# Kernel tuning notes

Hardware: AMD Instinct MI355X
Metric: run time of the kernel (lower is better)

The kernel has to match this reference:

```python
import jax, jax.numpy as jnp
import numpy as np

N_QUBITS = 7
N_LAYERS = 4
DIM = 2 ** N_QUBITS  # 128


def _cnot_perm(c, t, n=N_QUBITS):
    # PennyLane convention: wire 0 is the most-significant bit of the state index.
    idx = np.arange(2 ** n)
    ctrl = (idx >> (n - 1 - c)) & 1
    flipped = idx ^ (1 << (n - 1 - t))
    return np.where(ctrl == 1, flipped, idx)

# StronglyEntanglingLayers with a single layer uses range r=1: CNOT(j, (j+1) % n)
CNOT_PERMS = tuple(jnp.asarray(_cnot_perm(j, (j + 1) % N_QUBITS)) for j in range(N_QUBITS))

_bits = (np.arange(DIM)[None, :] >> (N_QUBITS - 1 - np.arange(N_QUBITS)[:, None])) & 1
Z_SIGNS = jnp.asarray(1.0 - 2.0 * _bits, dtype=jnp.float32)  # (7,128): +1 if wire bit 0 else -1


def _apply_1q(state, U, q):
    # state: (B,128) complex; U: (B,2,2) batched or (2,2) shared
    B = state.shape[0]
    s = state.reshape(B, 2 ** q, 2, 2 ** (N_QUBITS - 1 - q))
    if U.ndim == 3:
        s = jnp.einsum('bij,bpjq->bpiq', U, s)
    else:
        s = jnp.einsum('ij,bpjq->bpiq', U, s)
    return s.reshape(B, DIM)


def _simulate(x, weights):
    # x: (B,7) angles; weights: (4,7,3) Rot params. Returns <Z_q> per wire: (B,7)
    B = x.shape[0]
    state = jnp.zeros((B, DIM), jnp.complex64).at[:, 0].set(1.0)
    half = 0.5 * x
    c = jnp.cos(half).astype(jnp.complex64)  # (B,7)
    s = jnp.sin(half).astype(jnp.complex64)
    for l in range(N_LAYERS):
        # AngleEmbedding: RX(x_j) on wire j (data re-uploading, same x each block)
        for q in range(N_QUBITS):
            cq, sq = c[:, q], s[:, q]
            U = jnp.stack([jnp.stack([cq, -1j * sq], axis=-1),
                           jnp.stack([-1j * sq, cq], axis=-1)], axis=-2)  # (B,2,2)
            state = _apply_1q(state, U, q)
        # StronglyEntanglingLayers single layer: Rot(phi,theta,omega) per wire
        for q in range(N_QUBITS):
            phi, theta, omega = weights[l, q, 0], weights[l, q, 1], weights[l, q, 2]
            ct = jnp.cos(0.5 * theta).astype(jnp.complex64)
            st = jnp.sin(0.5 * theta).astype(jnp.complex64)
            ep = jnp.exp(-0.5j * (phi + omega).astype(jnp.complex64))
            em = jnp.exp(-0.5j * (phi - omega).astype(jnp.complex64))
            # Rot = RZ(omega) @ RY(theta) @ RZ(phi)
            U = jnp.stack([jnp.stack([ep * ct, -jnp.conj(em) * st]),
                           jnp.stack([em * st, jnp.conj(ep) * ct])])  # (2,2)
            state = _apply_1q(state, U, q)
        # entangler: CNOT(j, j+1 mod 7) for all j
        for q in range(N_QUBITS):
            state = state[:, CNOT_PERMS[q]]
    probs = state.real ** 2 + state.imag ** 2  # (B,128)
    return probs @ Z_SIGNS.T  # (B,7)


def setup_inputs() -> dict:
    key = jax.random.key(0)
    ks = jax.random.split(key, 6)
    B, n_classes = 16384, 22
    return {
        'x': jax.random.uniform(ks[0], (B, N_QUBITS), jnp.float32),
        'weights': jax.random.normal(ks[1], (N_LAYERS, N_QUBITS, 3), jnp.float32),
        'fc1_w': jax.random.normal(ks[2], (32, N_QUBITS), jnp.float32) * 0.3,
        'fc1_b': jax.random.normal(ks[3], (32,), jnp.float32) * 0.1,
        'fc2_w': jax.random.normal(ks[4], (n_classes, 32), jnp.float32) * 0.2,
        'fc2_b': jax.random.normal(ks[5], (n_classes,), jnp.float32) * 0.1,
    }


def reference(x, weights, fc1_w, fc1_b, fc2_w, fc2_b):
    q_out = _simulate(x, weights)                      # (B,7)
    h = jax.nn.relu(q_out @ fc1_w.T + fc1_b)           # (B,32); dropout is inference no-op
    return h @ fc2_w.T + fc2_b                         # (B,n_classes)
```

## Files before the change

### kernel.cpp

```cpp
#include <hip/hip_runtime.h>

constexpr int NQ = 7;
constexpr int NL = 4;
constexpr int NG = NL * NQ;
constexpr int NCLS = 22;
constexpr int EPB = 16;

typedef float v2 __attribute__((ext_vector_type(2)));
#define FMA2(a,b,c) __builtin_elementwise_fma((a),(b),(c))

__device__ __forceinline__ v2 sp(float s) { v2 r; r.x = s; r.y = s; return r; }
__device__ __forceinline__ v2 sel(bool c, v2 a, v2 b) {
    v2 r; r.x = c ? a.x : b.x; r.y = c ? a.y : b.y; return r;
}

template<int CTRL>
__device__ __forceinline__ float fdpp(float v) {
    return __int_as_float(__builtin_amdgcn_mov_dpp(__float_as_int(v), CTRL, 0xF, 0xF, true));
}
template<int OFF>
__device__ __forceinline__ float fswz(float v) {
    return __int_as_float(__builtin_amdgcn_ds_swizzle(__float_as_int(v), OFF));
}
template<int M>
__device__ __forceinline__ float xorl(float v) {
    if      constexpr (M == 1)  return fdpp<0xB1>(v);
    else if constexpr (M == 2)  return fdpp<0x4E>(v);
    else if constexpr (M == 4)  return fswz<0x101F>(v);
    else                        return fdpp<0x128>(v);
}
template<int M>
__device__ __forceinline__ v2 shufv(v2 v) {
    v2 r; r.x = xorl<M>(v.x); r.y = xorl<M>(v.y); return r;
}

__device__ __forceinline__ void fuse(const float* __restrict__ u, float c, float s,
                                     float4& A, float4& B) {
    A.x = fmaf(c, u[0],  s * u[3]);  A.y = fmaf(c, u[1], -s * u[2]);
    A.z = fmaf(c, u[2],  s * u[1]);  A.w = fmaf(c, u[3], -s * u[0]);
    B.x = fmaf(c, u[4],  s * u[7]);  B.y = fmaf(c, u[5], -s * u[6]);
    B.z = fmaf(c, u[6],  s * u[5]);  B.w = fmaf(c, u[7], -s * u[4]);
}

template<int M>
__device__ __forceinline__ void gateLane(int lane, float4 A, float4 B,
                                         v2 X[4], v2 Y[4]) {
    const bool hi = (lane & M) != 0;
    const float cvr = hi ? B.z : A.x, cvi = hi ? B.w : A.y;
    const float cwr = hi ? B.x : A.z, cwi = hi ? B.y : A.w;
    v2 Xs[4], Ys[4];
    #pragma unroll
    for (int j = 0; j < 4; ++j) { Xs[j] = shufv<M>(X[j]); Ys[j] = shufv<M>(Y[j]); }
    #pragma unroll
    for (int j = 0; j < 4; ++j) {
        v2 nX = FMA2(sp(cvr), X[j], FMA2(sp(-cvi), Y[j], FMA2(sp(cwr), Xs[j], sp(-cwi)*Ys[j])));
        v2 nY = FMA2(sp(cvr), Y[j], FMA2(sp( cvi), X[j], FMA2(sp(cwr), Ys[j], sp( cwi)*Xs[j])));
        X[j] = nX; Y[j] = nY;
    }
}

__device__ __forceinline__ void gateCross(float4 A, float4 B,
                                          v2& Xa, v2& Ya, v2& Xb, v2& Yb) {
    v2 nXa = FMA2(sp(A.x), Xa, FMA2(sp(-A.y), Ya, FMA2(sp(A.z), Xb, sp(-A.w)*Yb)));
    v2 nYa = FMA2(sp(A.x), Ya, FMA2(sp( A.y), Xa, FMA2(sp(A.z), Yb, sp( A.w)*Xb)));
    v2 nXb = FMA2(sp(B.x), Xa, FMA2(sp(-B.y), Ya, FMA2(sp(B.z), Xb, sp(-B.w)*Yb)));
    v2 nYb = FMA2(sp(B.x), Ya, FMA2(sp( B.y), Xa, FMA2(sp(B.z), Yb, sp( B.w)*Xb)));
    Xa = nXa; Ya = nYa; Xb = nXb; Yb = nYb;
}

__global__ __launch_bounds__(256) void reupload_kernel(
    const float* __restrict__ x,
    const float* __restrict__ wts,
    const float* __restrict__ fc1_w,
    const float* __restrict__ fc1_b,
    const float* __restrict__ fc2_w,
    const float* __restrict__ fc2_b,
    float* __restrict__ out,
    int B)
{
    __shared__ __align__(16) float rotU[NG * 8];
    __shared__ float2 csb[EPB * NQ];
    __shared__ __align__(16) float fU[NG * EPB * 8];
    __shared__ __align__(16) float fUT[NL * EPB * 8];
    __shared__ __align__(16) float hbuf[EPB][32];

    const int tid = threadIdx.x;
    if (tid < EPB * NQ) {
        const int e = tid / NQ, q = tid % NQ;
        const int bb = blockIdx.x * EPB + e;
        const float xv = (bb < B) ? x[bb*NQ + q] : 0.f;
        const float h = 0.5f * xv;
        csb[tid] = make_float2(__cosf(h), __sinf(h));
    } else if (tid >= 128 && tid < 128 + NG) {
        const int g = tid - 128;
        float phi = wts[g*3+0], th = wts[g*3+1], om = wts[g*3+2];
        float ct = __cosf(0.5f*th), st = __sinf(0.5f*th);
        float ap = 0.5f*(phi+om),  am = 0.5f*(phi-om);
        float cp = __cosf(ap), sp_ = __sinf(ap);
        float cm = __cosf(am), sm = __sinf(am);
        float* u = &rotU[g*8];
        u[0] =  cp*ct; u[1] = -sp_*ct;
        u[2] = -cm*st; u[3] = -sm*st;
        u[4] =  cm*st; u[5] = -sm*st;
        u[6] =  cp*ct; u[7] =  sp_*ct;
    }
    __syncthreads();
    #pragma unroll
    for (int i = tid; i < NG * EPB; i += 256) {
        const int g = i >> 4, e = i & 15;
        const int q = g % NQ;
        const float2 cs = csb[e*NQ + q];
        float4 A, Bq;
        fuse(&rotU[g*8], cs.x, cs.y, A, Bq);
        float4* dst = reinterpret_cast<float4*>(&fU[(g*EPB + e)*8]);
        dst[0] = A; dst[1] = Bq;
        if (q == 5) {
            const int l = g / NQ;
            float* td = &fUT[(l*EPB + e)*8];
            td[0] = A.x; td[1] = Bq.x; td[2] = A.y; td[3] = Bq.y;
            td[4] = A.z; td[5] = Bq.z; td[6] = A.w; td[7] = Bq.w;
        }
    }
    __syncthreads();

    const int lane = threadIdx.x & 63;
    const int u    = threadIdx.x & 15;
    const int grp  = threadIdx.x >> 4;
    const int b    = blockIdx.x * EPB + grp;
    if (b >= B) return;

    const int srcLane = (lane & 48) | ((u ^ (u >> 1)) & 15);

    v2 X[4], Y[4];
    #pragma unroll
    for (int j = 0; j < 4; ++j) { X[j] = sp(0.f); Y[j] = sp(0.f); }
    X[0].x = (u == 0) ? 1.f : 0.f;

    #pragma unroll
    for (int l = 0; l < NL; ++l) {
        float4 A, Bq;
        #define LOADU(q) { const float4* up = reinterpret_cast<const float4*>( \
            &fU[((l*NQ + (q))*EPB + grp)*8]); A = up[0]; Bq = up[1]; }
        LOADU(0); gateLane<8>(lane, A, Bq, X, Y);
        LOADU(1); gateLane<4>(lane, A, Bq, X, Y);
        LOADU(2); gateLane<2>(lane, A, Bq, X, Y);
        LOADU(3); gateLane<1>(lane, A, Bq, X, Y);
        LOADU(4);
        gateCross(A, Bq, X[0], Y[0], X[2], Y[2]);
        gateCross(A, Bq, X[1], Y[1], X[3], Y[3]);
        {
            const v2* tp = reinterpret_cast<const v2*>(&fUT[(l*EPB + grp)*8]);
            const v2 c00r = tp[0], c00i = tp[1], c01r = tp[2], c01i = tp[3];
            #pragma unroll
            for (int j = 0; j < 4; ++j) {
                const v2 Xxx = X[j].xx, Xyy = X[j].yy;
                const v2 Yxx = Y[j].xx, Yyy = Y[j].yy;
                v2 nX = FMA2(c00r, Xxx, FMA2(-c00i, Yxx, FMA2(c01r, Xyy, (-c01i)*Yyy)));
                v2 nY = FMA2(c00r, Yxx, FMA2( c00i, Xxx, FMA2(c01r, Yyy, ( c01i)*Xyy)));
                X[j] = nX; Y[j] = nY;
            }
        }
        LOADU(6);
        gateCross(A, Bq, X[0], Y[0], X[1], Y[1]);
        gateCross(A, Bq, X[2], Y[2], X[3], Y[3]);
        #undef LOADU

        #pragma unroll
        for (int j = 0; j < 4; ++j) {
            X[j].x = __shfl(X[j].x, srcLane); X[j].y = __shfl(X[j].y, srcLane);
            Y[j].x = __shfl(Y[j].x, srcLane); Y[j].y = __shfl(Y[j].y, srcLane);
        }
        {
            const bool cc = (lane & 1) != 0;
            v2 t;
            t = X[0]; X[0] = sel(cc, X[2], X[0]); X[2] = sel(cc, t, X[2]);
            t = X[1]; X[1] = sel(cc, X[3], X[1]); X[3] = sel(cc, t, X[3]);
            t = Y[0]; Y[0] = sel(cc, Y[2], Y[0]); Y[2] = sel(cc, t, Y[2]);
            t = Y[1]; Y[1] = sel(cc, Y[3], Y[1]); Y[3] = sel(cc, t, Y[3]);
        }
        {
            X[2] = X[2].yx; X[3] = X[3].yx; Y[2] = Y[2].yx; Y[3] = Y[3].yx;
        }
        {
            float t;
            t = X[0].y; X[0].y = X[1].y; X[1].y = t;
            t = X[2].y; X[2].y = X[3].y; X[3].y = t;
            t = Y[0].y; Y[0].y = Y[1].y; Y[1].y = t;
            t = Y[2].y; Y[2].y = Y[3].y; Y[3].y = t;
        }
        {
            X[1] = shufv<8>(X[1]); X[3] = shufv<8>(X[3]);
            Y[1] = shufv<8>(Y[1]); Y[3] = shufv<8>(Y[3]);
        }
    }

    v2 P[4];
    #pragma unroll
    for (int j = 0; j < 4; ++j) P[j] = FMA2(X[j], X[j], Y[j]*Y[j]);
    const v2 Sa = P[0] + P[1], Sb = P[2] + P[3];
    const v2 Se = P[0] + P[2], So = P[1] + P[3];
    const v2 T  = Sa + Sb;
    const float t = T.x + T.y;
    float z[NQ];
    z[0] = (lane & 8) ? -t : t;
    z[1] = (lane & 4) ? -t : t;
    z[2] = (lane & 2) ? -t : t;
    z[3] = (lane & 1) ? -t : t;
    z[4] = (Sa.x + Sa.y) - (Sb.x + Sb.y);
    z[5] = T.x - T.y;
    z[6] = (Se.x + Se.y) - (So.x + So.y);
    #pragma unroll
    for (int j = 0; j < NQ; ++j) {
        float v = z[j];
        v += xorl<1>(v);
        v += xorl<2>(v);
        const float q4  = fdpp<0x124>(v);
        const float q8  = fdpp<0x128>(v);
        const float q12 = fdpp<0x12C>(v);
        z[j] = (v + q8) + (q4 + q12);
    }

    float acc1a = fc1_b[u], acc1b = fc1_b[u + 16];
    #pragma unroll
    for (int j = 0; j < NQ; ++j) {
        acc1a = fmaf(z[j], fc1_w[u*NQ + j], acc1a);
        acc1b = fmaf(z[j], fc1_w[(u+16)*NQ + j], acc1b);
    }
    hbuf[grp][u]      = fmaxf(acc1a, 0.f);
    hbuf[grp][u + 16] = fmaxf(acc1b, 0.f);
    __builtin_amdgcn_wave_barrier();
    asm volatile("s_waitcnt lgkmcnt(0)" ::: "memory");
    __builtin_amdgcn_sched_barrier(0);

    float hv[32];
    #pragma unroll
    for (int i = 0; i < 8; ++i) {
        float4 v4 = *reinterpret_cast<const float4*>(&hbuf[grp][i*4]);
        hv[i*4+0] = v4.x; hv[i*4+1] = v4.y; hv[i*4+2] = v4.z; hv[i*4+3] = v4.w;
    }
    const int kb = (u < NCLS - 16) ? (u + 16) : 0;
    float acc2a = fc2_b[u], acc2b = fc2_b[kb];
    const float4* w4a = reinterpret_cast<const float4*>(fc2_w + u*32);
    const float4* w4b = reinterpret_cast<const float4*>(fc2_w + kb*32);
    #pragma unroll
    for (int i = 0; i < 8; ++i) {
        float4 wa = w4a[i], wb = w4b[i];
        acc2a = fmaf(hv[i*4+0], wa.x, acc2a); acc2b = fmaf(hv[i*4+0], wb.x, acc2b);
        acc2a = fmaf(hv[i*4+1], wa.y, acc2a); acc2b = fmaf(hv[i*4+1], wb.y, acc2b);
        acc2a = fmaf(hv[i*4+2], wa.z, acc2a); acc2b = fmaf(hv[i*4+2], wb.z, acc2b);
        acc2a = fmaf(hv[i*4+3], wa.w, acc2a); acc2b = fmaf(hv[i*4+3], wb.w, acc2b);
    }
    out[b*NCLS + u] = acc2a;
    if (u < NCLS - 16) out[b*NCLS + 16 + u] = acc2b;
}

extern "C" void kernel_launch(void* const* d_in, const int* in_sizes, int n_in,
                              void* d_out, int out_size, void* d_ws, size_t ws_size,
                              hipStream_t stream) {
    const float* x     = (const float*)d_in[0];
    const float* wts   = (const float*)d_in[1];
    const float* fc1_w = (const float*)d_in[2];
    const float* fc1_b = (const float*)d_in[3];
    const float* fc2_w = (const float*)d_in[4];
    const float* fc2_b = (const float*)d_in[5];
    float* out = (float*)d_out;

    const int B = in_sizes[0] / NQ;
    const int grid = (B + EPB - 1) / EPB;
    reupload_kernel<<<grid, 256, 0, stream>>>(x, wts, fc1_w, fc1_b, fc2_w, fc2_b, out, B);
}
```

Before: 20.12 us.

## Spread each 128-amplitude state over 32 lanes instead of 16

Each batch element's statevector now spans 32 lanes with 4 amplitudes per lane, down from 16 lanes with 8 amplitudes. Qubit 4 becomes a lane-level gate using a swizzle, the entangler permutation is adapted to 32 lanes, and the readout and MLP stages each use one output per lane. Blocks handle 8 elements, and a launch-bounds occupancy hint is added. This cuts per-thread register state and serial FMA chains in exchange for twice the threads per element, more cross-lane shuffles, and double the blocks with their per-block setup.

```diff
diff --git a/kernel.cpp b/kernel.cpp
--- a/kernel.cpp
+++ b/kernel.cpp
@@ -4,15 +4,12 @@
 constexpr int NL = 4;
 constexpr int NG = NL * NQ;
 constexpr int NCLS = 22;
-constexpr int EPB = 16;
+constexpr int EPB = 8;
 
 typedef float v2 __attribute__((ext_vector_type(2)));
 #define FMA2(a,b,c) __builtin_elementwise_fma((a),(b),(c))
 
 __device__ __forceinline__ v2 sp(float s) { v2 r; r.x = s; r.y = s; return r; }
-__device__ __forceinline__ v2 sel(bool c, v2 a, v2 b) {
-    v2 r; r.x = c ? a.x : b.x; r.y = c ? a.y : b.y; return r;
-}
 
 template<int CTRL>
 __device__ __forceinline__ float fdpp(float v) {
@@ -27,7 +24,8 @@
     if      constexpr (M == 1)  return fdpp<0xB1>(v);
     else if constexpr (M == 2)  return fdpp<0x4E>(v);
     else if constexpr (M == 4)  return fswz<0x101F>(v);
-    else                        return fdpp<0x128>(v);
+    else if constexpr (M == 8)  return fdpp<0x128>(v);
+    else                        return fswz<0x401F>(v);
 }
 template<int M>
 __device__ __forceinline__ v2 shufv(v2 v) {
@@ -44,15 +42,15 @@
 
 template<int M>
 __device__ __forceinline__ void gateLane(int lane, float4 A, float4 B,
-                                         v2 X[4], v2 Y[4]) {
+                                         v2 X[2], v2 Y[2]) {
     const bool hi = (lane & M) != 0;
     const float cvr = hi ? B.z : A.x, cvi = hi ? B.w : A.y;
     const float cwr = hi ? B.x : A.z, cwi = hi ? B.y : A.w;
-    v2 Xs[4], Ys[4];
-    #pragma unroll
-    for (int j = 0; j < 4; ++j) { Xs[j] = shufv<M>(X[j]); Ys[j] = shufv<M>(Y[j]); }
-    #pragma unroll
-    for (int j = 0; j < 4; ++j) {
+    v2 Xs[2], Ys[2];
+    #pragma unroll
+    for (int j = 0; j < 2; ++j) { Xs[j] = shufv<M>(X[j]); Ys[j] = shufv<M>(Y[j]); }
+    #pragma unroll
+    for (int j = 0; j < 2; ++j) {
         v2 nX = FMA2(sp(cvr), X[j], FMA2(sp(-cvi), Y[j], FMA2(sp(cwr), Xs[j], sp(-cwi)*Ys[j])));
         v2 nY = FMA2(sp(cvr), Y[j], FMA2(sp( cvi), X[j], FMA2(sp(cwr), Ys[j], sp( cwi)*Xs[j])));
         X[j] = nX; Y[j] = nY;
@@ -68,7 +66,7 @@
     Xa = nXa; Ya = nYa; Xb = nXb; Yb = nYb;
 }
 
-__global__ __launch_bounds__(256) void reupload_kernel(
+__global__ __launch_bounds__(256, 8) void reupload_kernel(
     const float* __restrict__ x,
     const float* __restrict__ wts,
     const float* __restrict__ fc1_w,
@@ -91,8 +89,8 @@
         const float xv = (bb < B) ? x[bb*NQ + q] : 0.f;
         const float h = 0.5f * xv;
         csb[tid] = make_float2(__cosf(h), __sinf(h));
-    } else if (tid >= 128 && tid < 128 + NG) {
-        const int g = tid - 128;
+    } else if (tid >= 64 && tid < 64 + NG) {
+        const int g = tid - 64;
         float phi = wts[g*3+0], th = wts[g*3+1], om = wts[g*3+2];
         float ct = __cosf(0.5f*th), st = __sinf(0.5f*th);
         float ap = 0.5f*(phi+om),  am = 0.5f*(phi-om);
@@ -105,9 +103,8 @@
         u[6] =  cp*ct; u[7] =  sp_*ct;
     }
     __syncthreads();
-    #pragma unroll
-    for (int i = tid; i < NG * EPB; i += 256) {
-        const int g = i >> 4, e = i & 15;
+    if (tid < NG * EPB) {
+        const int g = tid >> 3, e = tid & 7;
         const int q = g % NQ;
         const float2 cs = csb[e*NQ + q];
         float4 A, Bq;
@@ -124,35 +121,32 @@
     __syncthreads();
 
     const int lane = threadIdx.x & 63;
-    const int u    = threadIdx.x & 15;
-    const int grp  = threadIdx.x >> 4;
+    const int wl   = threadIdx.x & 31;
+    const int grp  = threadIdx.x >> 5;
     const int b    = blockIdx.x * EPB + grp;
     if (b >= B) return;
 
-    const int srcLane = (lane & 48) | ((u ^ (u >> 1)) & 15);
-
-    v2 X[4], Y[4];
-    #pragma unroll
-    for (int j = 0; j < 4; ++j) { X[j] = sp(0.f); Y[j] = sp(0.f); }
-    X[0].x = (u == 0) ? 1.f : 0.f;
+    const int srcLane = (lane & 32) | ((wl ^ (wl >> 1)) & 31);
+
+    v2 X[2], Y[2];
+    X[0] = sp(0.f); X[1] = sp(0.f); Y[0] = sp(0.f); Y[1] = sp(0.f);
+    X[0].x = (wl == 0) ? 1.f : 0.f;
 
     #pragma unroll
     for (int l = 0; l < NL; ++l) {
         float4 A, Bq;
         #define LOADU(q) { const float4* up = reinterpret_cast<const float4*>( \
             &fU[((l*NQ + (q))*EPB + grp)*8]); A = up[0]; Bq = up[1]; }
-        LOADU(0); gateLane<8>(lane, A, Bq, X, Y);
-        LOADU(1); gateLane<4>(lane, A, Bq, X, Y);
-        LOADU(2); gateLane<2>(lane, A, Bq, X, Y);
-        LOADU(3); gateLane<1>(lane, A, Bq, X, Y);
-        LOADU(4);
-        gateCross(A, Bq, X[0], Y[0], X[2], Y[2]);
-        gateCross(A, Bq, X[1], Y[1], X[3], Y[3]);
+        LOADU(0); gateLane<16>(lane, A, Bq, X, Y);
+        LOADU(1); gateLane< 8>(lane, A, Bq, X, Y);
+        LOADU(2); gateLane< 4>(lane, A, Bq, X, Y);
+        LOADU(3); gateLane< 2>(lane, A, Bq, X, Y);
+        LOADU(4); gateLane< 1>(lane, A, Bq, X, Y);
         {
             const v2* tp = reinterpret_cast<const v2*>(&fUT[(l*EPB + grp)*8]);
             const v2 c00r = tp[0], c00i = tp[1], c01r = tp[2], c01i = tp[3];
             #pragma unroll
-            for (int j = 0; j < 4; ++j) {
+            for (int j = 0; j < 2; ++j) {
                 const v2 Xxx = X[j].xx, Xyy = X[j].yy;
                 const v2 Yxx = Y[j].xx, Yyy = Y[j].yy;
                 v2 nX = FMA2(c00r, Xxx, FMA2(-c00i, Yxx, FMA2(c01r, Xyy, (-c01i)*Yyy)));
@@ -162,53 +156,46 @@
         }
         LOADU(6);
         gateCross(A, Bq, X[0], Y[0], X[1], Y[1]);
-        gateCross(A, Bq, X[2], Y[2], X[3], Y[3]);
         #undef LOADU
 
         #pragma unroll
-        for (int j = 0; j < 4; ++j) {
+        for (int j = 0; j < 2; ++j) {
             X[j].x = __shfl(X[j].x, srcLane); X[j].y = __shfl(X[j].y, srcLane);
             Y[j].x = __shfl(Y[j].x, srcLane); Y[j].y = __shfl(Y[j].y, srcLane);
         }
         {
             const bool cc = (lane & 1) != 0;
-            v2 t;
-            t = X[0]; X[0] = sel(cc, X[2], X[0]); X[2] = sel(cc, t, X[2]);
-            t = X[1]; X[1] = sel(cc, X[3], X[1]); X[3] = sel(cc, t, X[3]);
-            t = Y[0]; Y[0] = sel(cc, Y[2], Y[0]); Y[2] = sel(cc, t, Y[2]);
-            t = Y[1]; Y[1] = sel(cc, Y[3], Y[1]); Y[3] = sel(cc, t, Y[3]);
-        }
-        {
-            X[2] = X[2].yx; X[3] = X[3].yx; Y[2] = Y[2].yx; Y[3] = Y[3].yx;
+            #pragma unroll
+            for (int j = 0; j < 2; ++j) {
+                v2 xs = X[j].yx, ys = Y[j].yx;
+                X[j].x = cc ? xs.x : X[j].x;  X[j].y = cc ? xs.y : X[j].y;
+                Y[j].x = cc ? ys.x : Y[j].x;  Y[j].y = cc ? ys.y : Y[j].y;
+            }
         }
         {
             float t;
             t = X[0].y; X[0].y = X[1].y; X[1].y = t;
-            t = X[2].y; X[2].y = X[3].y; X[3].y = t;
             t = Y[0].y; Y[0].y = Y[1].y; Y[1].y = t;
-            t = Y[2].y; Y[2].y = Y[3].y; Y[3].y = t;
-        }
-        {
-            X[1] = shufv<8>(X[1]); X[3] = shufv<8>(X[3]);
-            Y[1] = shufv<8>(Y[1]); Y[3] = shufv<8>(Y[3]);
-        }
-    }
-
-    v2 P[4];
-    #pragma unroll
-    for (int j = 0; j < 4; ++j) P[j] = FMA2(X[j], X[j], Y[j]*Y[j]);
-    const v2 Sa = P[0] + P[1], Sb = P[2] + P[3];
-    const v2 Se = P[0] + P[2], So = P[1] + P[3];
-    const v2 T  = Sa + Sb;
+        }
+        {
+            X[1] = shufv<16>(X[1]);
+            Y[1] = shufv<16>(Y[1]);
+        }
+    }
+
+    v2 P[2];
+    #pragma unroll
+    for (int j = 0; j < 2; ++j) P[j] = FMA2(X[j], X[j], Y[j]*Y[j]);
+    const v2 T = P[0] + P[1];
     const float t = T.x + T.y;
     float z[NQ];
-    z[0] = (lane & 8) ? -t : t;
-    z[1] = (lane & 4) ? -t : t;
-    z[2] = (lane & 2) ? -t : t;
-    z[3] = (lane & 1) ? -t : t;
-    z[4] = (Sa.x + Sa.y) - (Sb.x + Sb.y);
+    z[0] = (lane & 16) ? -t : t;
+    z[1] = (lane &  8) ? -t : t;
+    z[2] = (lane &  4) ? -t : t;
+    z[3] = (lane &  2) ? -t : t;
+    z[4] = (lane &  1) ? -t : t;
     z[5] = T.x - T.y;
-    z[6] = (Se.x + Se.y) - (So.x + So.y);
+    z[6] = (P[0].x + P[0].y) - (P[1].x + P[1].y);
     #pragma unroll
     for (int j = 0; j < NQ; ++j) {
         float v = z[j];
@@ -217,17 +204,15 @@
         const float q4  = fdpp<0x124>(v);
         const float q8  = fdpp<0x128>(v);
         const float q12 = fdpp<0x12C>(v);
-        z[j] = (v + q8) + (q4 + q12);
-    }
-
-    float acc1a = fc1_b[u], acc1b = fc1_b[u + 16];
-    #pragma unroll
-    for (int j = 0; j < NQ; ++j) {
-        acc1a = fmaf(z[j], fc1_w[u*NQ + j], acc1a);
-        acc1b = fmaf(z[j], fc1_w[(u+16)*NQ + j], acc1b);
-    }
-    hbuf[grp][u]      = fmaxf(acc1a, 0.f);
-    hbuf[grp][u + 16] = fmaxf(acc1b, 0.f);
+        v = (v + q8) + (q4 + q12);
+        v += fswz<0x401F>(v);
+        z[j] = v;
+    }
+
+    float acc1 = fc1_b[wl];
+    #pragma unroll
+    for (int j = 0; j < NQ; ++j) acc1 = fmaf(z[j], fc1_w[wl*NQ + j], acc1);
+    hbuf[grp][wl] = fmaxf(acc1, 0.f);
     __builtin_amdgcn_wave_barrier();
     asm volatile("s_waitcnt lgkmcnt(0)" ::: "memory");
     __builtin_amdgcn_sched_barrier(0);
@@ -238,20 +223,18 @@
         float4 v4 = *reinterpret_cast<const float4*>(&hbuf[grp][i*4]);
         hv[i*4+0] = v4.x; hv[i*4+1] = v4.y; hv[i*4+2] = v4.z; hv[i*4+3] = v4.w;
     }
-    const int kb = (u < NCLS - 16) ? (u + 16) : 0;
-    float acc2a = fc2_b[u], acc2b = fc2_b[kb];
-    const float4* w4a = reinterpret_cast<const float4*>(fc2_w + u*32);
-    const float4* w4b = reinterpret_cast<const float4*>(fc2_w + kb*32);
+    const int k = (wl < NCLS) ? wl : 0;
+    float acc2 = fc2_b[k];
+    const float4* w4 = reinterpret_cast<const float4*>(fc2_w + k*32);
     #pragma unroll
     for (int i = 0; i < 8; ++i) {
-        float4 wa = w4a[i], wb = w4b[i];
-        acc2a = fmaf(hv[i*4+0], wa.x, acc2a); acc2b = fmaf(hv[i*4+0], wb.x, acc2b);
-        acc2a = fmaf(hv[i*4+1], wa.y, acc2a); acc2b = fmaf(hv[i*4+1], wb.y, acc2b);
-        acc2a = fmaf(hv[i*4+2], wa.z, acc2a); acc2b = fmaf(hv[i*4+2], wb.z, acc2b);
-        acc2a = fmaf(hv[i*4+3], wa.w, acc2a); acc2b = fmaf(hv[i*4+3], wb.w, acc2b);
-    }
-    out[b*NCLS + u] = acc2a;
-    if (u < NCLS - 16) out[b*NCLS + 16 + u] = acc2b;
+        float4 wv = w4[i];
+        acc2 = fmaf(hv[i*4+0], wv.x, acc2);
+        acc2 = fmaf(hv[i*4+1], wv.y, acc2);
+        acc2 = fmaf(hv[i*4+2], wv.z, acc2);
+        acc2 = fmaf(hv[i*4+3], wv.w, acc2);
+    }
+    if (wl < NCLS) out[b*NCLS + wl] = acc2;
 }
 
 extern "C" void kernel_launch(void* const* d_in, const int* in_sizes, int n_in,
```

Measured after the change: 21.49 us. 6.8% more time.
